# Performance work log

Measured on AMD Instinct MI355X. Metric: run time of the kernel, lower is better.

## Reference

```python
import jax, jax.numpy as jnp
import numpy as np
import math

B, S, HID = 1, 2048, 4096
HQ, HKV, D = 32, 8, 128
G = HQ // HKV          # GQA group size
OBS, W, SINK = 128, 32, 2
THETA = 500000.0
TOP_FRAC, MID_SPARSITY, LOW_FRAC = 0.05, 0.7, 0.20
K_KEEP = int(math.ceil((1.0 - MID_SPARSITY) * D))  # elements kept per level-1 token


def _rope(x):
    # x: [B, H, S, D]; standard Llama rotary embedding
    half = D // 2
    inv_freq = 1.0 / (THETA ** (jnp.arange(half, dtype=jnp.float32) / half))
    ang = jnp.arange(S, dtype=jnp.float32)[:, None] * inv_freq[None, :]  # [S, half]
    cos = jnp.concatenate([jnp.cos(ang), jnp.cos(ang)], axis=-1)  # [S, D]
    sin = jnp.concatenate([jnp.sin(ang), jnp.sin(ang)], axis=-1)
    x1, x2 = x[..., :half], x[..., half:]
    rot = jnp.concatenate([-x2, x1], axis=-1)
    return x * cos[None, None] + rot * sin[None, None]


def _topk_mask(x):
    # keep the K_KEEP largest-magnitude elements of each length-D token vector
    a = jnp.abs(x)
    thr = jnp.sort(a, axis=-1)[..., D - K_KEEP]
    return a >= thr[..., None]


def setup_inputs() -> dict:
    key = jax.random.key(0)
    ks = jax.random.split(key, 5)
    sc = HID ** -0.5
    return {
        "hidden_states": jax.random.normal(ks[0], (B, S, HID), dtype=jnp.float32),
        "wq": jax.random.normal(ks[1], (HID, HQ * D), dtype=jnp.float32) * sc,
        "wk": jax.random.normal(ks[2], (HID, HKV * D), dtype=jnp.float32) * sc,
        "wv": jax.random.normal(ks[3], (HID, HKV * D), dtype=jnp.float32) * sc,
        "wo": jax.random.normal(ks[4], (HQ * D, HID), dtype=jnp.float32) * sc,
    }


def reference(hidden_states, wq, wk, wv, wo):
    scale = 1.0 / math.sqrt(D)
    q = (hidden_states @ wq).reshape(B, S, HQ, D).transpose(0, 2, 1, 3)   # [B,HQ,S,D]
    k = (hidden_states @ wk).reshape(B, S, HKV, D).transpose(0, 2, 1, 3)  # [B,HKV,S,D]
    v = (hidden_states @ wv).reshape(B, S, HKV, D).transpose(0, 2, 1, 3)
    q, k = _rope(q), _rope(k)

    # --- observation-window GQA attention (grouped queries vs all keys) ---
    obs_q = q[:, :, S - OBS:, :].reshape(B, HKV, G, OBS, D)
    s_obs = jnp.einsum('bhgqd,bhkd->bhgqk', obs_q, k) * scale
    obs_causal = jnp.arange(S)[None, :] <= (S - OBS + jnp.arange(OBS))[:, None]  # [OBS,S]
    s_obs = jnp.where(obs_causal[None, None, None], s_obs, -jnp.inf)
    aw_kv = jax.nn.softmax(s_obs.astype(jnp.float32), axis=-1).mean(axis=2)  # [B,HKV,OBS,S]

    # per-token importance, normalized by how many obs queries observed each key
    counts = jnp.minimum(OBS, S - jnp.arange(S)).astype(jnp.float32)
    imp = aw_kv.sum(axis=2) / counts[None, None, :]  # [B,HKV,S]

    # --- global thresholds over the compressible region -> 3 sparsity levels ---
    imp_c = imp[:, :, :S - W].reshape(-1)
    t_high = jnp.quantile(imp_c, 1.0 - TOP_FRAC)
    t_low = jnp.quantile(imp_c, LOW_FRAC)
    level = jnp.where(imp >= t_high, 0, jnp.where(imp < t_low, 2, 1))
    pos = jnp.arange(S)
    dense_pos = (pos >= S - W) | (pos < SINK)     # recent window + sinks stay dense
    level = jnp.where(dense_pos[None, None, :], 0, level)

    keep_k = jnp.where((level == 0)[..., None], True, (level == 1)[..., None] & _topk_mask(k))
    keep_v = jnp.where((level == 0)[..., None], True, (level == 1)[..., None] & _topk_mask(v))
    k_sp = k * keep_k
    v_sp = v * keep_v
    evicted = level == 2

    # --- causal GQA attention over the sparsified KV cache ---
    q_g = q.reshape(B, HKV, G, S, D)
    s = jnp.einsum('bhgqd,bhkd->bhgqk', q_g, k_sp) * scale
    causal = jnp.tril(jnp.ones((S, S), dtype=bool))
    allow = causal[None, None, None] & (~evicted)[:, :, None, None, :]
    s = jnp.where(allow, s, -jnp.inf)
    p = jax.nn.softmax(s.astype(jnp.float32), axis=-1).astype(v_sp.dtype)
    o = jnp.einsum('bhgqk,bhkd->bhgqd', p, v_sp)
    o = o.reshape(B, HQ, S, D).transpose(0, 2, 1, 3).reshape(B, S, HQ * D)
    return o @ wo
```

## Files before the change

### kernel.cpp

```cpp
#include <hip/hip_runtime.h>
#include <hip/hip_bf16.h>
#include <math.h>

#define S_    2048
#define HID_  4096
#define HQ_   32
#define HKV_  8
#define D_    128
#define G_    4
#define OBS_  128
#define W_    32
#define NKV_  1024
#define NQ_   4096
#define KLD_  2048
#define SCALE_ 0.08838834764831845f
#define THR_IDX_ 89
#define NC_   16128

typedef __attribute__((ext_vector_type(4))) float f32x4;
typedef __attribute__((ext_vector_type(8))) short s16x8;
typedef __attribute__((ext_vector_type(8))) unsigned short u16x8;
typedef __attribute__((ext_vector_type(4))) unsigned short u16x4;
typedef unsigned short ushort_t;

struct TermPtrs { const ushort_t* a[6]; const ushort_t* b[6]; };
struct M1A { const ushort_t* A[3]; const ushort_t* B[3];
             const ushort_t* QA[3]; const ushort_t* QB[3]; };

__device__ __forceinline__ unsigned short f2bf(float x) {
  union { float f; unsigned u; } v; v.f = x;
  unsigned r = v.u + 0x7FFFu + ((v.u >> 16) & 1u);
  return (unsigned short)(r >> 16);
}
__device__ __forceinline__ float bf2f(unsigned short b) {
  union { unsigned u; float f; } v; v.u = ((unsigned)b) << 16;
  return v.f;
}
__device__ __forceinline__ void gload_lds16(const void* g, void* l) {
  __builtin_amdgcn_global_load_lds((const __attribute__((address_space(1))) unsigned int*)g,
                                   (__attribute__((address_space(3))) unsigned int*)l, 16, 0, 0);
}
__device__ __forceinline__ void term_sel(const TermPtrs& P, int tt,
                                         const ushort_t*& As, const ushort_t*& Bs) {
  switch (tt) {
    case 0: As = P.a[0]; Bs = P.b[0]; break;
    case 1: As = P.a[1]; Bs = P.b[1]; break;
    case 2: As = P.a[2]; Bs = P.b[2]; break;
    case 3: As = P.a[3]; Bs = P.b[3]; break;
    case 4: As = P.a[4]; Bs = P.b[4]; break;
    default: As = P.a[5]; Bs = P.b[5]; break;
  }
}
__device__ __forceinline__ void xcd_bmbn(int& bm, int& bn) {
  int nplane = gridDim.x * gridDim.y;
  int l = blockIdx.y * gridDim.x + blockIdx.x;
  int v = (l & 7) * (nplane >> 3) + (l >> 3);
  bm = v / gridDim.x;
  bn = v - bm * gridDim.x;
}

__device__ __forceinline__ void splitT_body(const float* __restrict__ src, int N,
                                            ushort_t* __restrict__ t0,
                                            ushort_t* __restrict__ t1,
                                            ushort_t* __restrict__ t2,
                                            int idx, float (*tile)[65]) {
  const int t = threadIdx.x;
  const int ntx = N >> 6;
  const int n0 = (idx % ntx) * 64, k0 = (idx / ntx) * 64;
#pragma unroll
  for (int i = 0; i < 16; ++i) {
    int s = i * 256 + t;
    int r = s >> 6, c = s & 63;
    tile[r][c] = src[(size_t)(k0 + r) * N + n0 + c];
  }
  __syncthreads();
#pragma unroll
  for (int i = 0; i < 16; ++i) {
    int s = i * 256 + t;
    int n = s >> 6, kk = s & 63;
    float x = tile[kk][n];
    unsigned short b0 = f2bf(x);
    size_t o = (size_t)(n0 + n) * HID_ + k0 + kk;
    t0[o] = b0;
    if (t1) {
      float r = x - bf2f(b0);
      unsigned short b1 = f2bf(r);
      t1[o] = b1;
      t2[o] = f2bf(r - bf2f(b1));
    }
  }
}

__global__ __launch_bounds__(256) void prep_kernel(const float* __restrict__ hid,
                                                   const float* __restrict__ wq,
                                                   const float* __restrict__ wk,
                                                   const float* __restrict__ wv,
                                                   ushort_t* h0, ushort_t* h1, ushort_t* h2,
                                                   ushort_t* wq0T, ushort_t* wq1T, ushort_t* wq2T,
                                                   ushort_t* wkv0T, ushort_t* wkv1T, ushort_t* wkv2T,
                                                   float* invf) {
  __shared__ float tile[64][65];
  const int b = blockIdx.x;
  if (b < 8192) {
    int idx = b * 256 + threadIdx.x;
    float4 v = ((const float4*)hid)[idx];
    u16x4 o0, o1, o2;
    float xs[4] = {v.x, v.y, v.z, v.w};
#pragma unroll
    for (int e = 0; e < 4; ++e) {
      float x = xs[e];
      unsigned short b0 = f2bf(x);
      float r = x - bf2f(b0);
      unsigned short b1 = f2bf(r);
      o0[e] = b0; o1[e] = b1; o2[e] = f2bf(r - bf2f(b1));
    }
    *(u16x4*)(h0 + (size_t)idx * 4) = o0;
    *(u16x4*)(h1 + (size_t)idx * 4) = o1;
    *(u16x4*)(h2 + (size_t)idx * 4) = o2;
  } else if (b < 12288) {
    splitT_body(wq, NQ_, wq0T, wq1T, wq2T, b - 8192, tile);
  } else if (b < 13312) {
    splitT_body(wk, NKV_, wkv0T, wkv1T, wkv2T, b - 12288, tile);
  } else if (b < 14336) {
    splitT_body(wv, NKV_, wkv0T + (size_t)NKV_ * HID_, wkv1T + (size_t)NKV_ * HID_,
                wkv2T + (size_t)NKV_ * HID_, b - 13312, tile);
  } else {
    int j = threadIdx.x;
    if (j < 64) invf[j] = (float)(1.0 / pow(500000.0, (double)j / 64.0));
  }
}

__global__ __launch_bounds__(256) void gemm6m(M1A P, float* __restrict__ kvp,
                                              float* __restrict__ qpart) {
  __shared__ ushort_t lds[6 * 128 * 32];
  const int t = threadIdx.x;
  const int wave = t >> 6, lane = t & 63;
  const int lc = lane & 15, lg = lane >> 4;
  const int wm = wave >> 1, wn = wave & 1;
  const int z = blockIdx.z;

  const ushort_t *As0, *As1, *As2, *Bs0, *Bs1, *Bs2;
  float* C;
  int rowA, rowB, kbeg, ksteps, N, crow0, ccol0;
  if (z < 2) {
    int bm, bn;
    xcd_bmbn(bm, bn);
    As0 = P.A[0]; As1 = P.A[1]; As2 = P.A[2];
    Bs0 = P.B[0]; Bs1 = P.B[1]; Bs2 = P.B[2];
    rowA = bm * 128; rowB = bn * 128;
    kbeg = z * 64; ksteps = 64; N = KLD_;
    C = kvp + (size_t)z * S_ * KLD_;
    crow0 = bm * 128; ccol0 = bn * 128;
  } else {
    int l = blockIdx.y * gridDim.x + blockIdx.x;
    int bn = l & 31, ks = l >> 5;
    As0 = P.QA[0]; As1 = P.QA[1]; As2 = P.QA[2];
    Bs0 = P.QB[0]; Bs1 = P.QB[1]; Bs2 = P.QB[2];
    rowA = 0; rowB = bn * 128;
    kbeg = ks * 16; ksteps = 16; N = NQ_;
    C = qpart + (size_t)ks * 128 * NQ_;
    crow0 = 0; ccol0 = bn * 128;
  }

  f32x4 acc[4][4];
#pragma unroll
  for (int fi = 0; fi < 4; ++fi)
#pragma unroll
    for (int fj = 0; fj < 4; ++fj) acc[fi][fj] = 0.f;

  for (int kb = kbeg; kb < kbeg + ksteps; ++kb) {
    __syncthreads();
#pragma unroll
    for (int ti = 0; ti < 6; ++ti) {
      const ushort_t* src = (ti == 0) ? As0 : (ti == 1) ? As1 : (ti == 2) ? As2
                          : (ti == 3) ? Bs0 : (ti == 4) ? Bs1 : Bs2;
      const int rb = (ti < 3) ? rowA : rowB;
#pragma unroll
      for (int it = 0; it < 2; ++it) {
        int slot = it * 256 + t;
        int row = slot >> 2, cp = slot & 3;
        int c = (cp - (row >> 1)) & 3;
        gload_lds16(src + (size_t)(rb + row) * HID_ + kb * 32 + c * 8,
                    lds + ti * 4096 + it * 2048 + wave * 512);
      }
    }
    __syncthreads();
    s16x8 a0[4], a1[4], a2[4], bfr[4];
#pragma unroll
    for (int f = 0; f < 4; ++f) {
      int ra = wm * 64 + f * 16 + lc;
      int ca = ((lg + (ra >> 1)) & 3) * 8;
      a0[f] = *(const s16x8*)(lds + 0 * 4096 + ra * 32 + ca);
      a1[f] = *(const s16x8*)(lds + 1 * 4096 + ra * 32 + ca);
      a2[f] = *(const s16x8*)(lds + 2 * 4096 + ra * 32 + ca);
    }
#pragma unroll
    for (int f = 0; f < 4; ++f) {
      int rb2 = wn * 64 + f * 16 + lc;
      bfr[f] = *(const s16x8*)(lds + 3 * 4096 + rb2 * 32 + (((lg + (rb2 >> 1)) & 3) * 8));
    }
#pragma unroll
    for (int fi = 0; fi < 4; ++fi)
#pragma unroll
      for (int fj = 0; fj < 4; ++fj) {
        acc[fi][fj] = __builtin_amdgcn_mfma_f32_16x16x32_bf16(a0[fi], bfr[fj], acc[fi][fj], 0, 0, 0);
        acc[fi][fj] = __builtin_amdgcn_mfma_f32_16x16x32_bf16(a1[fi], bfr[fj], acc[fi][fj], 0, 0, 0);
        acc[fi][fj] = __builtin_amdgcn_mfma_f32_16x16x32_bf16(a2[fi], bfr[fj], acc[fi][fj], 0, 0, 0);
      }
#pragma unroll
    for (int f = 0; f < 4; ++f) {
      int rb2 = wn * 64 + f * 16 + lc;
      bfr[f] = *(const s16x8*)(lds + 4 * 4096 + rb2 * 32 + (((lg + (rb2 >> 1)) & 3) * 8));
    }
#pragma unroll
    for (int fi = 0; fi < 4; ++fi)
#pragma unroll
      for (int fj = 0; fj < 4; ++fj) {
        acc[fi][fj] = __builtin_amdgcn_mfma_f32_16x16x32_bf16(a0[fi], bfr[fj], acc[fi][fj], 0, 0, 0);
        acc[fi][fj] = __builtin_amdgcn_mfma_f32_16x16x32_bf16(a1[fi], bfr[fj], acc[fi][fj], 0, 0, 0);
      }
#pragma unroll
    for (int f = 0; f < 4; ++f) {
      int rb2 = wn * 64 + f * 16 + lc;
      bfr[f] = *(const s16x8*)(lds + 5 * 4096 + rb2 * 32 + (((lg + (rb2 >> 1)) & 3) * 8));
    }
#pragma unroll
    for (int fi = 0; fi < 4; ++fi)
#pragma unroll
      for (int fj = 0; fj < 4; ++fj)
        acc[fi][fj] = __builtin_amdgcn_mfma_f32_16x16x32_bf16(a0[fi], bfr[fj], acc[fi][fj], 0, 0, 0);
  }
#pragma unroll
  for (int fi = 0; fi < 4; ++fi)
#pragma unroll
    for (int fj = 0; fj < 4; ++fj)
#pragma unroll
      for (int r = 0; r < 4; ++r)
        C[(size_t)(crow0 + wm * 64 + fi * 16 + lg * 4 + r) * N +
          ccol0 + wn * 64 + fj * 16 + lc] = acc[fi][fj][r];
}

__device__ __forceinline__ void gemm1_body(const ushort_t* __restrict__ A,
                                           const ushort_t* __restrict__ B,
                                           float* __restrict__ C,
                                           int N, int K, int KSTEPS, ushort_t* lds) {
  const int t = threadIdx.x;
  const int wave = t >> 6, lane = t & 63;
  const int lc = lane & 15, lg = lane >> 4;
  int bm, bn;
  xcd_bmbn(bm, bn);
  const int wm = wave >> 1, wn = wave & 1;
  const int srow = t >> 3, schunk = t & 7;

  f32x4 acc[4][4];
#pragma unroll
  for (int fi = 0; fi < 4; ++fi)
#pragma unroll
    for (int fj = 0; fj < 4; ++fj) acc[fi][fj] = 0.f;

  for (int kb = 0; kb < KSTEPS; ++kb) {
    __syncthreads();
#pragma unroll
    for (int g = 0; g < 4; ++g) {
      int row = g * 32 + srow;
      int sw = schunk ^ (row & 7);
      size_t co = kb * 64 + sw * 8;
      gload_lds16(A + (size_t)(bm * 128 + row) * K + co, lds + g * 2048 + wave * 512);
      gload_lds16(B + (size_t)(bn * 128 + row) * K + co, lds + 8192 + g * 2048 + wave * 512);
    }
    __syncthreads();
#pragma unroll
    for (int ks = 0; ks < 2; ++ks) {
      s16x8 af[4], bf[4];
#pragma unroll
      for (int f = 0; f < 4; ++f) {
        int ra = wm * 64 + f * 16 + lc;
        af[f] = *(const s16x8*)(lds + ra * 64 + (((ks * 4 + lg) ^ (ra & 7)) * 8));
        int rb = wn * 64 + f * 16 + lc;
        bf[f] = *(const s16x8*)(lds + 8192 + rb * 64 + (((ks * 4 + lg) ^ (rb & 7)) * 8));
      }
#pragma unroll
      for (int fi = 0; fi < 4; ++fi)
#pragma unroll
        for (int fj = 0; fj < 4; ++fj)
          acc[fi][fj] = __builtin_amdgcn_mfma_f32_16x16x32_bf16(af[fi], bf[fj], acc[fi][fj], 0, 0, 0);
    }
  }
#pragma unroll
  for (int fi = 0; fi < 4; ++fi)
#pragma unroll
    for (int fj = 0; fj < 4; ++fj)
#pragma unroll
      for (int r = 0; r < 4; ++r)
        C[(size_t)(bm * 128 + wm * 64 + fi * 16 + lg * 4 + r) * N +
          bn * 128 + wn * 64 + fj * 16 + lc] = acc[fi][fj][r];
}

__global__ __launch_bounds__(256) void gemm1(const ushort_t* __restrict__ A,
                                             const ushort_t* __restrict__ B,
                                             float* __restrict__ C,
                                             int N, int K, int KSTEPS) {
  __shared__ ushort_t lds[2 * 128 * 64];
  gemm1_body(A, B, C, N, K, KSTEPS, lds);
}

__device__ __forceinline__ void gemm_qrope_body(const ushort_t* __restrict__ A,
                                                const ushort_t* __restrict__ B,
                                                ushort_t* __restrict__ qb16,
                                                const float* __restrict__ invf,
                                                ushort_t* lds) {
  const int t = threadIdx.x;
  const int wave = t >> 6, lane = t & 63;
  const int lc = lane & 15, lg = lane >> 4;
  int bm, bn;
  xcd_bmbn(bm, bn);
  const int srow = t >> 3, schunk = t & 7;

  f32x4 acc[2][8];
#pragma unroll
  for (int f = 0; f < 2; ++f)
#pragma unroll
    for (int fj = 0; fj < 8; ++fj) acc[f][fj] = 0.f;

  for (int kb = 0; kb < 64; ++kb) {
    __syncthreads();
#pragma unroll
    for (int g = 0; g < 4; ++g) {
      int row = g * 32 + srow;
      int sw = schunk ^ (row & 7);
      size_t co = (size_t)kb * 64 + sw * 8;
      gload_lds16(A + (size_t)(bm * 128 + row) * HID_ + co, lds + g * 2048 + wave * 512);
      gload_lds16(B + (size_t)(bn * 128 + row) * HID_ + co, lds + 8192 + g * 2048 + wave * 512);
    }
    __syncthreads();
#pragma unroll
    for (int ks = 0; ks < 2; ++ks) {
      s16x8 af[2], bf[8];
#pragma unroll
      for (int f = 0; f < 2; ++f) {
        int ra = wave * 32 + f * 16 + lc;
        af[f] = *(const s16x8*)(lds + ra * 64 + (((ks * 4 + lg) ^ (ra & 7)) * 8));
      }
#pragma unroll
      for (int fj = 0; fj < 8; ++fj) {
        int rb = fj * 16 + lc;
        bf[fj] = *(const s16x8*)(lds + 8192 + rb * 64 + (((ks * 4 + lg) ^ (rb & 7)) * 8));
      }
#pragma unroll
      for (int f = 0; f < 2; ++f)
#pragma unroll
        for (int fj = 0; fj < 8; ++fj)
          acc[f][fj] = __builtin_amdgcn_mfma_f32_16x16x32_bf16(af[f], bf[fj], acc[f][fj], 0, 0, 0);
    }
  }
#pragma unroll
  for (int f = 0; f < 2; ++f)
#pragma unroll
    for (int r = 0; r < 4; ++r) {
      int row = bm * 128 + wave * 32 + f * 16 + lg * 4 + r;
      ushort_t* op = qb16 + (size_t)row * NQ_ + bn * 128;
#pragma unroll
      for (int fj = 0; fj < 4; ++fj) {
        int j = fj * 16 + lc;
        float x1 = acc[f][fj][r];
        float x2 = acc[f][fj + 4][r];
        float ang = (float)row * invf[j];
        float sn, cs; sincosf(ang, &sn, &cs);
        op[j] = f2bf(x1 * cs - x2 * sn);
        op[j + 64] = f2bf(x2 * cs + x1 * sn);
      }
    }
}

__global__ __launch_bounds__(256) void m2_kernel(const ushort_t* __restrict__ h0,
                                                 const ushort_t* __restrict__ wq0T,
                                                 ushort_t* __restrict__ qb16,
                                                 const float* __restrict__ kvp,
                                                 const float* __restrict__ invf,
                                                 float* __restrict__ kvf,
                                                 ushort_t* __restrict__ k0,
                                                 ushort_t* __restrict__ k1,
                                                 ushort_t* __restrict__ k2,
                                                 const float* __restrict__ qpart,
                                                 ushort_t* __restrict__ q0,
                                                 ushort_t* __restrict__ q1,
                                                 ushort_t* __restrict__ q2,
                                                 const float* __restrict__ wo,
                                                 ushort_t* __restrict__ woT) {
  __shared__ ushort_t lds[2 * 128 * 64];
  if (blockIdx.z == 0) {
    gemm_qrope_body(h0, wq0T, qb16, invf, lds);
    return;
  }
  const int l = blockIdx.y * gridDim.x + blockIdx.x;
  const int t = threadIdx.x;
  const size_t n = (size_t)S_ * KLD_;
  for (int vb = l; vb < 6144; vb += 512) {
    if (vb < 4096) {
      int idx = vb * 256 + t;
      int j = idx & 63;
      int h = (idx >> 6) & 7;
      int s = idx >> 9;
      size_t base = (size_t)s * KLD_ + h * 128 + j;
      float x1 = kvp[base] + kvp[base + n];
      float x2 = kvp[base + 64] + kvp[base + 64 + n];
      float ang = (float)s * invf[j];
      float sn, cs; sincosf(ang, &sn, &cs);
      float o1 = x1 * cs - x2 * sn;
      float o2 = x2 * cs + x1 * sn;
      kvf[base] = o1; kvf[base + 64] = o2;
      size_t o = (size_t)h * 262144 + (size_t)s * 128 + j;
      float ys[2] = {o1, o2};
#pragma unroll
      for (int e = 0; e < 2; ++e) {
        float x = ys[e];
        unsigned short b0 = f2bf(x);
        float r = x - bf2f(b0);
        unsigned short b1 = f2bf(r);
        k0[o + e * 64] = b0; k1[o + e * 64] = b1; k2[o + e * 64] = f2bf(r - bf2f(b1));
      }
    } else {
      int idx = (vb - 4096) * 256 + t;
      int s = idx >> 8, c4 = idx & 255;
      size_t base = (size_t)s * KLD_ + 1024 + c4 * 4;
      float4 a = *(const float4*)(kvp + base);
      float4 bb = *(const float4*)(kvp + base + n);
      float4 o;
      o.x = a.x + bb.x; o.y = a.y + bb.y; o.z = a.z + bb.z; o.w = a.w + bb.w;
      *(float4*)(kvf + base) = o;
    }
  }
  for (int vb = l; vb < 1024; vb += 512) {
    int idx = vb * 256 + t;
    int j = idx & 63;
    int hq = (idx >> 6) & 31;
    int i = idx >> 11;
    size_t base = (size_t)i * NQ_ + hq * 128 + j;
    float x1 = 0.f, x2 = 0.f;
#pragma unroll
    for (int z = 0; z < 8; ++z) {
      x1 += qpart[(size_t)z * OBS_ * NQ_ + base];
      x2 += qpart[(size_t)z * OBS_ * NQ_ + base + 64];
    }
    float ang = (float)(S_ - OBS_ + i) * invf[j];
    float sn, cs; sincosf(ang, &sn, &cs);
    float o1 = x1 * cs - x2 * sn;
    float o2 = x2 * cs + x1 * sn;
    int hk = hq >> 2, g = hq & 3;
    size_t o = (size_t)hk * 65536 + (size_t)(g * 128 + i) * 128 + j;
    float ys[2] = {o1, o2};
#pragma unroll
    for (int e = 0; e < 2; ++e) {
      float x = ys[e];
      unsigned short b0 = f2bf(x);
      float r = x - bf2f(b0);
      unsigned short b1 = f2bf(r);
      q0[o + e * 64] = b0; q1[o + e * 64] = b1; q2[o + e * 64] = f2bf(r - bf2f(b1));
    }
  }
  float (*tile)[65] = (float(*)[65])lds;
  for (int vb = l; vb < 4096; vb += 512) {
    __syncthreads();
    splitT_body(wo, HID_, woT, nullptr, nullptr, vb, tile);
  }
}

__global__ __launch_bounds__(256) void gemm6z(TermPtrs P, float* __restrict__ Cg) {
  __shared__ ushort_t lds[2 * 128 * 64];
  const int t = threadIdx.x;
  const int wave = t >> 6, lane = t & 63;
  const int lc = lane & 15, lg = lane >> 4;
  const int bm = blockIdx.y, bn = blockIdx.x, z = blockIdx.z;
  const int wm = wave >> 1, wn = wave & 1;
  const int srow = t >> 3, schunk = t & 7;
  const size_t Aoff = (size_t)z * 512 * 128;
  const size_t Boff = (size_t)z * 2048 * 128;
  float* C = Cg + (size_t)z * 512 * 2048;

  f32x4 acc[4][4];
#pragma unroll
  for (int fi = 0; fi < 4; ++fi)
#pragma unroll
    for (int fj = 0; fj < 4; ++fj) acc[fi][fj] = 0.f;

  for (int tt = 0; tt < 6; ++tt) {
    const ushort_t *As, *Bs;
    term_sel(P, tt, As, Bs);
    As += Aoff; Bs += Boff;
    for (int kb = 0; kb < 2; ++kb) {
      __syncthreads();
#pragma unroll
      for (int g = 0; g < 4; ++g) {
        int row = g * 32 + srow;
        int sw = schunk ^ (row & 7);
        gload_lds16(As + (size_t)(bm * 128 + row) * 128 + kb * 64 + sw * 8,
                    lds + g * 2048 + wave * 512);
        gload_lds16(Bs + (size_t)(bn * 128 + row) * 128 + kb * 64 + sw * 8,
                    lds + 8192 + g * 2048 + wave * 512);
      }
      __syncthreads();
#pragma unroll
      for (int ks = 0; ks < 2; ++ks) {
        s16x8 af[4], bf[4];
#pragma unroll
        for (int f = 0; f < 4; ++f) {
          int ra = wm * 64 + f * 16 + lc;
          af[f] = *(const s16x8*)(lds + ra * 64 + (((ks * 4 + lg) ^ (ra & 7)) * 8));
          int rb = wn * 64 + f * 16 + lc;
          bf[f] = *(const s16x8*)(lds + 8192 + rb * 64 + (((ks * 4 + lg) ^ (rb & 7)) * 8));
        }
#pragma unroll
        for (int fi = 0; fi < 4; ++fi)
#pragma unroll
          for (int fj = 0; fj < 4; ++fj)
            acc[fi][fj] = __builtin_amdgcn_mfma_f32_16x16x32_bf16(af[fi], bf[fj], acc[fi][fj], 0, 0, 0);
      }
    }
  }
#pragma unroll
  for (int fi = 0; fi < 4; ++fi)
#pragma unroll
    for (int fj = 0; fj < 4; ++fj)
#pragma unroll
      for (int r = 0; r < 4; ++r)
        C[(size_t)(bm * 128 + wm * 64 + fi * 16 + lg * 4 + r) * 2048 +
          bn * 128 + wn * 64 + fj * 16 + lc] = acc[fi][fj][r];
}

__global__ __launch_bounds__(256) void rowstat_kernel(const float* __restrict__ s,
                                                      float* __restrict__ mx,
                                                      float* __restrict__ dinv) {
  const int row = blockIdx.x * 4 + (threadIdx.x >> 6);
  const int lane = threadIdx.x & 63;
  const int i = row & 127;
  const int jmax = S_ - OBS_ + i;
  const float* sp = s + (size_t)row * S_;
  float vals[32];
  float m = -INFINITY;
#pragma unroll
  for (int c = 0; c < 8; ++c) {
    int j0 = c * 256 + lane * 4;
    float4 v = *(const float4*)(sp + j0);
    float e0 = (j0 + 0 <= jmax) ? v.x * SCALE_ : -INFINITY;
    float e1 = (j0 + 1 <= jmax) ? v.y * SCALE_ : -INFINITY;
    float e2 = (j0 + 2 <= jmax) ? v.z * SCALE_ : -INFINITY;
    float e3 = (j0 + 3 <= jmax) ? v.w * SCALE_ : -INFINITY;
    vals[c * 4 + 0] = e0; vals[c * 4 + 1] = e1; vals[c * 4 + 2] = e2; vals[c * 4 + 3] = e3;
    m = fmaxf(m, fmaxf(fmaxf(e0, e1), fmaxf(e2, e3)));
  }
#pragma unroll
  for (int off = 1; off < 64; off <<= 1) m = fmaxf(m, __shfl_xor(m, off, 64));
  float ssum = 0.f;
#pragma unroll
  for (int c = 0; c < 32; ++c) ssum += expf(vals[c] - m);
#pragma unroll
  for (int off = 1; off < 64; off <<= 1) ssum += __shfl_xor(ssum, off, 64);
  if (lane == 0) { mx[row] = m; dinv[row] = 1.0f / ssum; }
}

__global__ __launch_bounds__(256) void colsum_part(const float* __restrict__ s,
                                                   const float* __restrict__ mx,
                                                   const float* __restrict__ dinv,
                                                   float* __restrict__ part) {
  __shared__ float mxl[64], dvl[64];
  const int jt = blockIdx.x, hk = blockIdx.y, rc = blockIdx.z;
  const int t = threadIdx.x;
  if (t < 64) {
    mxl[t] = mx[hk * 512 + rc * 64 + t];
    dvl[t] = dinv[hk * 512 + rc * 64 + t];
  }
  __syncthreads();
  const int j = jt * 256 + t;
  const float* sp = s + ((size_t)hk * 512 + rc * 64) * S_ + j;
  float acc = 0.f;
  for (int rr = 0; rr < 64; ++rr) {
    int i = (rc * 64 + rr) & 127;
    if (j <= S_ - OBS_ + i)
      acc += expf(sp[(size_t)rr * S_] * SCALE_ - mxl[rr]) * dvl[rr];
  }
  part[((size_t)rc * 8 + hk) * S_ + j] = acc;
}

__global__ __launch_bounds__(1024) void radix_all(const float* __restrict__ part,
                                                  float* __restrict__ imp,
                                                  float* __restrict__ thr) {
  __shared__ unsigned hist[4][256];
  __shared__ unsigned pfx_s[4], need_s[4];
  const int t = threadIdx.x;
  for (int idx = t; idx < HKV_ * S_; idx += 1024) {
    int hk = idx >> 11, j = idx & 2047;
    float acc = 0.f;
#pragma unroll
    for (int rc = 0; rc < 8; ++rc) acc += part[((size_t)rc * 8 + hk) * S_ + j];
    float cnt = (float)min(OBS_, S_ - j);
    imp[idx] = acc * 0.25f / cnt;
  }
  if (t < 4) {
    pfx_s[t] = 0u;
    need_s[t] = (t == 0) ? 3225u : (t == 1) ? 3226u : (t == 2) ? 15320u : 15321u;
  }
  __syncthreads();
  for (int pass = 0; pass < 4; ++pass) {
    ((unsigned*)hist)[t] = 0u;
    __syncthreads();
    int shift = 24 - pass * 8;
    for (int idx = t; idx < NC_; idx += 1024) {
      int h = idx / (S_ - W_), j = idx - h * (S_ - W_);
      union { float f; unsigned u; } cv; cv.f = imp[h * S_ + j];
      unsigned u = cv.u;
#pragma unroll
      for (int q = 0; q < 4; ++q) {
        bool m = (pass == 0) || ((u >> (shift + 8)) == (pfx_s[q] >> (shift + 8)));
        if (m) atomicAdd(&hist[q][(u >> shift) & 255u], 1u);
      }
    }
    __syncthreads();
    if (t < 4) {
      unsigned need = need_s[t], cum = 0, pfx = pfx_s[t];
      for (int d = 0; d < 256; ++d) {
        unsigned c = hist[t][d];
        if (cum + c > need) { pfx |= ((unsigned)d) << shift; need_s[t] = need - cum; break; }
        cum += c;
      }
      pfx_s[t] = pfx;
    }
    __syncthreads();
  }
  if (t == 0) {
    union { unsigned u; float f; } c0, c1, c2, c3;
    c0.u = pfx_s[0]; c1.u = pfx_s[1]; c2.u = pfx_s[2]; c3.u = pfx_s[3];
    double fl = 0.2 * (double)(NC_ - 1) - 3225.0;
    double fh = 0.95 * (double)(NC_ - 1) - 15320.0;
    thr[0] = (float)((double)c2.f + ((double)c3.f - (double)c2.f) * fh);
    thr[1] = (float)((double)c0.f + ((double)c1.f - (double)c0.f) * fl);
  }
}

__global__ __launch_bounds__(128) void sparsify_kernel(const float* __restrict__ kv,
                                                       const float* __restrict__ imp,
                                                       const float* __restrict__ thr,
                                                       ushort_t* __restrict__ ksp,
                                                       ushort_t* __restrict__ vsp,
                                                       float* __restrict__ ebias) {
  const int b = blockIdx.x;
  const int j = b >> 3;
  const int h = b & 7;
  const int t = threadIdx.x;
  float ipv = imp[h * S_ + j];
  bool dense = (j >= S_ - W_) || (j < 2);
  int lvl = dense ? 0 : ((ipv >= thr[0]) ? 0 : ((ipv < thr[1]) ? 2 : 1));
  if (t == 0) ebias[h * S_ + j] = (lvl == 2) ? -INFINITY : 0.0f;
  __shared__ float av[128];
  __shared__ float thv;
  size_t base_in = (size_t)j * KLD_ + h * D_;
  size_t base_out = (size_t)j * NKV_ + h * D_;
  float kvv = kv[base_in + t];
  av[t] = fabsf(kvv);
  __syncthreads();
  {
    float at = av[t]; int cnt = 0;
    for (int m = 0; m < 128; ++m) { float am = av[m]; cnt += (am < at) || (am == at && m < t); }
    if (cnt == THR_IDX_) thv = at;
  }
  __syncthreads();
  {
    bool keep = (lvl == 0) || (lvl == 1 && fabsf(kvv) >= thv);
    ksp[base_out + t] = f2bf(keep ? kvv : 0.0f);
  }
  __syncthreads();
  float vvv = kv[base_in + 1024 + t];
  av[t] = fabsf(vvv);
  __syncthreads();
  {
    float at = av[t]; int cnt = 0;
    for (int m = 0; m < 128; ++m) { float am = av[m]; cnt += (am < at) || (am == at && m < t); }
    if (cnt == THR_IDX_) thv = at;
  }
  __syncthreads();
  {
    bool keep = (lvl == 0) || (lvl == 1 && fabsf(vvv) >= thv);
    vsp[base_out + t] = f2bf(keep ? vvv : 0.0f);
  }
}

__global__ __launch_bounds__(256) void vtrans_kernel(const ushort_t* __restrict__ vsp,
                                                     ushort_t* __restrict__ vspT) {
  __shared__ ushort_t tl[64][136];
  const int jt = blockIdx.x;
  const int hk = blockIdx.y;
  const int t = threadIdx.x;
#pragma unroll
  for (int i = 0; i < 4; ++i) {
    int idx = i * 256 + t;
    int j = idx >> 4, c = idx & 15;
    *(u16x8*)&tl[j][c * 8] = *(const u16x8*)(vsp + (size_t)(jt * 64 + j) * NKV_ + hk * 128 + c * 8);
  }
  __syncthreads();
  int d = t >> 1, j0 = (t & 1) * 32;
#pragma unroll
  for (int jj = 0; jj < 4; ++jj) {
    u16x8 v;
#pragma unroll
    for (int e = 0; e < 8; ++e) v[e] = tl[j0 + jj * 8 + e][d];
    *(u16x8*)(vspT + ((size_t)hk * 128 + d) * S_ + jt * 64 + j0 + jj * 8) = v;
  }
}

#define SPAD_ 66
__global__ __launch_bounds__(256) void attn_kernel(const ushort_t* __restrict__ qbp,
                                                   const ushort_t* __restrict__ ksp,
                                                   const ushort_t* __restrict__ vspT,
                                                   const float* __restrict__ ebias,
                                                   ushort_t* __restrict__ ob16) {
  __shared__ ushort_t k_lds[64 * 128];
  __shared__ ushort_t vT_lds[128 * 64];
  __shared__ float s_lds[4][16][SPAD_];
  const int b = blockIdx.x;
  const int xcd = b & 7;
  const int idx = b >> 3;
  const int h = xcd * 4 + (idx >> 4);
  const int p = idx & 15;
  const int hk = h >> 2;
  const int t = threadIdx.x;
  const int w = t >> 6, lane = t & 63;
  const int lc = lane & 15, lg = lane >> 4;

  const ushort_t* kbase = ksp + hk * D_;
  const ushort_t* vbase = vspT + (size_t)hk * D_ * S_;

  for (int strip = 0; strip < 2; ++strip) {
    const int qb = (strip == 0) ? p : 31 - p;
    const int q0 = qb * 64 + w * 16;
    s16x8 qfrag[4];
#pragma unroll
    for (int db = 0; db < 4; ++db)
      qfrag[db] = *(const s16x8*)(qbp + (size_t)(q0 + lc) * NQ_ + h * D_ + db * 32 + lg * 8);

    f32x4 o[8];
#pragma unroll
    for (int n = 0; n < 8; ++n) o[n] = 0.f;
    float mr[4] = {-INFINITY, -INFINITY, -INFINITY, -INFINITY};
    float lr[4] = {0.f, 0.f, 0.f, 0.f};

    const int ntj = qb + 1;
    for (int tj = 0; tj < ntj; ++tj) {
      const int j0 = tj * 64;
      __syncthreads();
#pragma unroll
      for (int i = 0; i < 4; ++i) {
        int slot = i * 256 + w * 64 + lane;
        int row = slot >> 4, c = slot & 15;
        const ushort_t* gp = kbase + (size_t)(j0 + row) * NKV_ + ((c ^ (row & 7)) * 8);
        gload_lds16(gp, &k_lds[(i * 256 + w * 64) * 8]);
      }
#pragma unroll
      for (int i = 0; i < 4; ++i) {
        int slot = i * 256 + w * 64 + lane;
        int d = slot >> 3, c = slot & 7;
        const ushort_t* gp = vbase + (size_t)d * S_ + j0 + ((c ^ (d & 7)) * 8);
        gload_lds16(gp, &vT_lds[(i * 256 + w * 64) * 8]);
      }
      __syncthreads();

      f32x4 sfr[4];
#pragma unroll
      for (int js = 0; js < 4; ++js) sfr[js] = 0.f;
#pragma unroll
      for (int js = 0; js < 4; ++js) {
        int row = js * 16 + lc;
#pragma unroll
        for (int db = 0; db < 4; ++db) {
          s16x8 kf = *(const s16x8*)&k_lds[row * 128 + (((db * 4 + lg) ^ (lc & 7)) * 8)];
          sfr[js] = __builtin_amdgcn_mfma_f32_16x16x32_bf16(qfrag[db], kf, sfr[js], 0, 0, 0);
        }
      }
      float eb[4];
#pragma unroll
      for (int js = 0; js < 4; ++js) eb[js] = ebias[hk * S_ + j0 + js * 16 + lc];

      const bool diag = (tj == qb);
      float sclv[4];
#pragma unroll
      for (int r = 0; r < 4; ++r) {
        float sv[4];
#pragma unroll
        for (int js = 0; js < 4; ++js) sv[js] = sfr[js][r] * SCALE_ + eb[js];
        if (diag) {
          int qrow = w * 16 + lg * 4 + r;
#pragma unroll
          for (int js = 0; js < 4; ++js)
            if (js * 16 + lc > qrow) sv[js] = -INFINITY;
        }
        float tm = fmaxf(fmaxf(sv[0], sv[1]), fmaxf(sv[2], sv[3]));
#pragma unroll
        for (int off = 1; off < 16; off <<= 1) tm = fmaxf(tm, __shfl_xor(tm, off, 64));
        float mnew = fmaxf(mr[r], tm);
        float scl = __expf(mr[r] - mnew);
        float ps = 0.f;
#pragma unroll
        for (int js = 0; js < 4; ++js) {
          float e = __expf(sv[js] - mnew);
          s_lds[w][lg * 4 + r][js * 16 + lc] = e;
          ps += e;
        }
#pragma unroll
        for (int off = 1; off < 16; off <<= 1) ps += __shfl_xor(ps, off, 64);
        lr[r] = lr[r] * scl + ps;
        mr[r] = mnew;
        sclv[r] = scl;
      }
#pragma unroll
      for (int n = 0; n < 8; ++n) {
        f32x4 ov = o[n];
#pragma unroll
        for (int r = 0; r < 4; ++r) ov[r] *= sclv[r];
        o[n] = ov;
      }
      asm volatile("s_waitcnt lgkmcnt(0)" ::: "memory");
      s16x8 pa[2];
#pragma unroll
      for (int ks = 0; ks < 2; ++ks) {
        float pv[8];
        *(f32x4*)&pv[0] = *(const f32x4*)&s_lds[w][lc][ks * 32 + lg * 8];
        *(f32x4*)&pv[4] = *(const f32x4*)&s_lds[w][lc][ks * 32 + lg * 8 + 4];
        s16x8 pk;
#pragma unroll
        for (int e = 0; e < 8; ++e) pk[e] = (short)f2bf(pv[e]);
        pa[ks] = pk;
      }
#pragma unroll
      for (int n = 0; n < 8; ++n) {
        int d = n * 16 + lc;
#pragma unroll
        for (int ks = 0; ks < 2; ++ks) {
          s16x8 vf = *(const s16x8*)&vT_lds[d * 64 + (((ks * 4 + lg) ^ (lc & 7)) * 8)];
          o[n] = __builtin_amdgcn_mfma_f32_16x16x32_bf16(pa[ks], vf, o[n], 0, 0, 0);
        }
      }
    }
#pragma unroll
    for (int r = 0; r < 4; ++r) {
      float rinv = 1.0f / lr[r];
      int row = q0 + lg * 4 + r;
#pragma unroll
      for (int n = 0; n < 8; ++n)
        ob16[(size_t)row * NQ_ + h * D_ + n * 16 + lc] = f2bf(o[n][r] * rinv);
    }
  }
}

extern "C" void kernel_launch(void* const* d_in, const int* in_sizes, int n_in,
                              void* d_out, int out_size, void* d_ws, size_t ws_size,
                              hipStream_t stream) {
  (void)in_sizes; (void)n_in; (void)out_size; (void)ws_size;
  const float* hid = (const float*)d_in[0];
  const float* wq  = (const float*)d_in[1];
  const float* wk  = (const float*)d_in[2];
  const float* wv  = (const float*)d_in[3];
  const float* wo  = (const float*)d_in[4];
  float* out = (float*)d_out;
  char* ws = (char*)d_ws;
  const size_t MB = 1ull << 20;

  ushort_t* h0     = (ushort_t*)(ws + 0 * MB);
  ushort_t* h1     = (ushort_t*)(ws + 16 * MB);
  ushort_t* h2     = (ushort_t*)(ws + 32 * MB);
  ushort_t* wq0T   = (ushort_t*)(ws + 48 * MB);
  ushort_t* wq1T   = (ushort_t*)(ws + 80 * MB);
  ushort_t* wq2T   = (ushort_t*)(ws + 112 * MB);
  ushort_t* wkv0T  = (ushort_t*)(ws + 144 * MB);
  ushort_t* wkv1T  = (ushort_t*)(ws + 160 * MB);
  ushort_t* wkv2T  = (ushort_t*)(ws + 176 * MB);
  float*    kvp    = (float*)d_out;
  float*    qpart  = (float*)(ws + 192 * MB);
  float*    kvf    = (float*)(ws + 112 * MB);
  ushort_t* qb16   = (ushort_t*)(ws + 16 * MB);
  ushort_t* kb0    = (ushort_t*)(ws + 32 * MB);
  ushort_t* kb1    = (ushort_t*)(ws + 36 * MB);
  ushort_t* kb2    = (ushort_t*)(ws + 40 * MB);
  float*    s_obs  = (float*)(ws + 48 * MB);
  ushort_t* woT    = (ushort_t*)(ws + 144 * MB);
  ushort_t* ksp    = (ushort_t*)(ws + 176 * MB);
  ushort_t* vsp    = (ushort_t*)(ws + 180 * MB);
  ushort_t* vspT   = (ushort_t*)(ws + 184 * MB);
  ushort_t* ob16   = (ushort_t*)(ws + 188 * MB + 512 * 1024);
  ushort_t* qo0    = (ushort_t*)(ws + 208 * MB);
  ushort_t* qo1    = (ushort_t*)(ws + 209 * MB);
  ushort_t* qo2    = (ushort_t*)(ws + 210 * MB);
  char*     misc   = ws + 212 * MB;
  float*    impv   = (float*)(misc + 0);
  float*    eb     = (float*)(misc + 64 * 1024);
  float*    invf   = (float*)(misc + 128 * 1024);
  float*    thr    = (float*)(misc + 132 * 1024);
  float*    part   = (float*)(misc + 256 * 1024);
  float*    mxbuf  = (float*)(misc + 1024 * 1024);
  float*    dinvb  = (float*)(misc + 1088 * 1024);

  prep_kernel<<<14337, 256, 0, stream>>>(hid, wq, wk, wv, h0, h1, h2,
                                         wq0T, wq1T, wq2T, wkv0T, wkv1T, wkv2T, invf);

  const size_t obs_off = (size_t)(S_ - OBS_) * HID_;
  {
    M1A P;
    P.A[0] = h0; P.A[1] = h1; P.A[2] = h2;
    P.B[0] = wkv0T; P.B[1] = wkv1T; P.B[2] = wkv2T;
    P.QA[0] = h0 + obs_off; P.QA[1] = h1 + obs_off; P.QA[2] = h2 + obs_off;
    P.QB[0] = wq0T; P.QB[1] = wq1T; P.QB[2] = wq2T;
    gemm6m<<<dim3(16, 16, 3), 256, 0, stream>>>(P, kvp, qpart);
  }

  m2_kernel<<<dim3(32, 16, 2), 256, 0, stream>>>(h0, wq0T, qb16, kvp, invf, kvf,
                                                 kb0, kb1, kb2, qpart, qo0, qo1, qo2,
                                                 wo, woT);

  {
    TermPtrs P;
    P.a[0] = qo0; P.b[0] = kb0;
    P.a[1] = qo0; P.b[1] = kb1;
    P.a[2] = qo1; P.b[2] = kb0;
    P.a[3] = qo1; P.b[3] = kb1;
    P.a[4] = qo0; P.b[4] = kb2;
    P.a[5] = qo2; P.b[5] = kb0;
    gemm6z<<<dim3(16, 4, 8), 256, 0, stream>>>(P, s_obs);
  }

  rowstat_kernel<<<1024, 256, 0, stream>>>(s_obs, mxbuf, dinvb);
  colsum_part<<<dim3(8, 8, 8), 256, 0, stream>>>(s_obs, mxbuf, dinvb, part);
  radix_all<<<1, 1024, 0, stream>>>(part, impv, thr);

  sparsify_kernel<<<S_ * HKV_, 128, 0, stream>>>(kvf, impv, thr, ksp, vsp, eb);
  vtrans_kernel<<<dim3(S_ / 64, HKV_), 256, 0, stream>>>(vsp, vspT);
  attn_kernel<<<512, 256, 0, stream>>>(qb16, ksp, vspT, eb, ob16);

  gemm1<<<dim3(32, 16, 1), 256, 0, stream>>>(ob16, woT, out, HID_, HID_, 64);
}
```

Measured before the change: 812.5 us.

## Move Q projection+RoPE into gemm6m, drop KV split-K, add MFMA priority hints

The Q projection with RoPE moves out of the second kernel and into the first GEMM launch as extra z-slices, so it runs alongside the KV projection. The KV GEMM no longer splits K across two partial buffers; each block does the full reduction, which removes the partial-sum add and the V-copy pass in the finish kernel. Sparsify now reads V straight from the projection output, and qb16 is placed in the output buffer. The attention kernel wraps its MFMA loops in s_setprio hints. The risk is load imbalance from longer KV blocks mixed with the much heavier Q blocks in one grid.

After: 832.0 us. 1.02x slower.

```diff
diff --git a/kernel.cpp b/kernel.cpp
--- a/kernel.cpp
+++ b/kernel.cpp
@@ -131,25 +131,90 @@
 }
 
 __global__ __launch_bounds__(256) void gemm6m(M1A P, float* __restrict__ kvp,
-                                              float* __restrict__ qpart) {
+                                              float* __restrict__ qpart,
+                                              ushort_t* __restrict__ qb16,
+                                              const float* __restrict__ invf) {
   __shared__ ushort_t lds[6 * 128 * 32];
   const int t = threadIdx.x;
   const int wave = t >> 6, lane = t & 63;
   const int lc = lane & 15, lg = lane >> 4;
+  const int z = blockIdx.z;
+
+  if (z >= 2) {
+    int tid = (z - 2) * 256 + blockIdx.y * gridDim.x + blockIdx.x;
+    int v = (tid & 7) * 64 + (tid >> 3);
+    int bm = v >> 5, bn = v & 31;
+    const ushort_t* A = P.A[0];
+    const ushort_t* B = P.QB[0];
+    const int srow = t >> 3, schunk = t & 7;
+    f32x4 acc[2][8];
+#pragma unroll
+    for (int f = 0; f < 2; ++f)
+#pragma unroll
+      for (int fj = 0; fj < 8; ++fj) acc[f][fj] = 0.f;
+    for (int kb = 0; kb < 64; ++kb) {
+      __syncthreads();
+#pragma unroll
+      for (int g = 0; g < 4; ++g) {
+        int row = g * 32 + srow;
+        int sw = schunk ^ (row & 7);
+        size_t co = (size_t)kb * 64 + sw * 8;
+        gload_lds16(A + (size_t)(bm * 128 + row) * HID_ + co, lds + g * 2048 + wave * 512);
+        gload_lds16(B + (size_t)(bn * 128 + row) * HID_ + co, lds + 8192 + g * 2048 + wave * 512);
+      }
+      __syncthreads();
+#pragma unroll
+      for (int ks = 0; ks < 2; ++ks) {
+        s16x8 af[2], bf[8];
+#pragma unroll
+        for (int f = 0; f < 2; ++f) {
+          int ra = wave * 32 + f * 16 + lc;
+          af[f] = *(const s16x8*)(lds + ra * 64 + (((ks * 4 + lg) ^ (ra & 7)) * 8));
+        }
+#pragma unroll
+        for (int fj = 0; fj < 8; ++fj) {
+          int rb = fj * 16 + lc;
+          bf[fj] = *(const s16x8*)(lds + 8192 + rb * 64 + (((ks * 4 + lg) ^ (rb & 7)) * 8));
+        }
+#pragma unroll
+        for (int f = 0; f < 2; ++f)
+#pragma unroll
+          for (int fj = 0; fj < 8; ++fj)
+            acc[f][fj] = __builtin_amdgcn_mfma_f32_16x16x32_bf16(af[f], bf[fj], acc[f][fj], 0, 0, 0);
+      }
+    }
+#pragma unroll
+    for (int f = 0; f < 2; ++f)
+#pragma unroll
+      for (int r = 0; r < 4; ++r) {
+        int row = bm * 128 + wave * 32 + f * 16 + lg * 4 + r;
+        ushort_t* op = qb16 + (size_t)row * NQ_ + bn * 128;
+#pragma unroll
+        for (int fj = 0; fj < 4; ++fj) {
+          int j = fj * 16 + lc;
+          float x1 = acc[f][fj][r];
+          float x2 = acc[f][fj + 4][r];
+          float ang = (float)row * invf[j];
+          float sn, cs; sincosf(ang, &sn, &cs);
+          op[j] = f2bf(x1 * cs - x2 * sn);
+          op[j + 64] = f2bf(x2 * cs + x1 * sn);
+        }
+      }
+    return;
+  }
+
   const int wm = wave >> 1, wn = wave & 1;
-  const int z = blockIdx.z;
-
   const ushort_t *As0, *As1, *As2, *Bs0, *Bs1, *Bs2;
   float* C;
   int rowA, rowB, kbeg, ksteps, N, crow0, ccol0;
-  if (z < 2) {
+  if (z == 0) {
     int bm, bn;
     xcd_bmbn(bm, bn);
     As0 = P.A[0]; As1 = P.A[1]; As2 = P.A[2];
     Bs0 = P.B[0]; Bs1 = P.B[1]; Bs2 = P.B[2];
     rowA = bm * 128; rowB = bn * 128;
-    kbeg = z * 64; ksteps = 64; N = KLD_;
-    C = kvp + (size_t)z * S_ * KLD_;
+    kbeg = 0; ksteps = 128; N = KLD_;
+    C = kvp;
     crow0 = bm * 128; ccol0 = bn * 128;
   } else {
     int l = blockIdx.y * gridDim.x + blockIdx.x;
@@ -240,10 +305,11 @@
           ccol0 + wn * 64 + fj * 16 + lc] = acc[fi][fj][r];
 }
 
-__device__ __forceinline__ void gemm1_body(const ushort_t* __restrict__ A,
-                                           const ushort_t* __restrict__ B,
-                                           float* __restrict__ C,
-                                           int N, int K, int KSTEPS, ushort_t* lds) {
+__global__ __launch_bounds__(256) void gemm1(const ushort_t* __restrict__ A,
+                                             const ushort_t* __restrict__ B,
+                                             float* __restrict__ C,
+                                             int N, int K, int KSTEPS) {
+  __shared__ ushort_t lds[2 * 128 * 64];
   const int t = threadIdx.x;
   const int wave = t >> 6, lane = t & 63;
   const int lc = lane & 15, lg = lane >> 4;
@@ -296,138 +362,43 @@
           bn * 128 + wn * 64 + fj * 16 + lc] = acc[fi][fj][r];
 }
 
-__global__ __launch_bounds__(256) void gemm1(const ushort_t* __restrict__ A,
-                                             const ushort_t* __restrict__ B,
-                                             float* __restrict__ C,
-                                             int N, int K, int KSTEPS) {
-  __shared__ ushort_t lds[2 * 128 * 64];
-  gemm1_body(A, B, C, N, K, KSTEPS, lds);
-}
-
-__device__ __forceinline__ void gemm_qrope_body(const ushort_t* __restrict__ A,
-                                                const ushort_t* __restrict__ B,
-                                                ushort_t* __restrict__ qb16,
-                                                const float* __restrict__ invf,
-                                                ushort_t* lds) {
-  const int t = threadIdx.x;
-  const int wave = t >> 6, lane = t & 63;
-  const int lc = lane & 15, lg = lane >> 4;
-  int bm, bn;
-  xcd_bmbn(bm, bn);
-  const int srow = t >> 3, schunk = t & 7;
-
-  f32x4 acc[2][8];
-#pragma unroll
-  for (int f = 0; f < 2; ++f)
-#pragma unroll
-    for (int fj = 0; fj < 8; ++fj) acc[f][fj] = 0.f;
-
-  for (int kb = 0; kb < 64; ++kb) {
-    __syncthreads();
-#pragma unroll
-    for (int g = 0; g < 4; ++g) {
-      int row = g * 32 + srow;
-      int sw = schunk ^ (row & 7);
-      size_t co = (size_t)kb * 64 + sw * 8;
-      gload_lds16(A + (size_t)(bm * 128 + row) * HID_ + co, lds + g * 2048 + wave * 512);
-      gload_lds16(B + (size_t)(bn * 128 + row) * HID_ + co, lds + 8192 + g * 2048 + wave * 512);
-    }
-    __syncthreads();
-#pragma unroll
-    for (int ks = 0; ks < 2; ++ks) {
-      s16x8 af[2], bf[8];
-#pragma unroll
-      for (int f = 0; f < 2; ++f) {
-        int ra = wave * 32 + f * 16 + lc;
-        af[f] = *(const s16x8*)(lds + ra * 64 + (((ks * 4 + lg) ^ (ra & 7)) * 8));
-      }
-#pragma unroll
-      for (int fj = 0; fj < 8; ++fj) {
-        int rb = fj * 16 + lc;
-        bf[fj] = *(const s16x8*)(lds + 8192 + rb * 64 + (((ks * 4 + lg) ^ (rb & 7)) * 8));
-      }
-#pragma unroll
-      for (int f = 0; f < 2; ++f)
-#pragma unroll
-        for (int fj = 0; fj < 8; ++fj)
-          acc[f][fj] = __builtin_amdgcn_mfma_f32_16x16x32_bf16(af[f], bf[fj], acc[f][fj], 0, 0, 0);
-    }
-  }
-#pragma unroll
-  for (int f = 0; f < 2; ++f)
-#pragma unroll
-    for (int r = 0; r < 4; ++r) {
-      int row = bm * 128 + wave * 32 + f * 16 + lg * 4 + r;
-      ushort_t* op = qb16 + (size_t)row * NQ_ + bn * 128;
-#pragma unroll
-      for (int fj = 0; fj < 4; ++fj) {
-        int j = fj * 16 + lc;
-        float x1 = acc[f][fj][r];
-        float x2 = acc[f][fj + 4][r];
-        float ang = (float)row * invf[j];
-        float sn, cs; sincosf(ang, &sn, &cs);
-        op[j] = f2bf(x1 * cs - x2 * sn);
-        op[j + 64] = f2bf(x2 * cs + x1 * sn);
-      }
-    }
-}
-
-__global__ __launch_bounds__(256) void m2_kernel(const ushort_t* __restrict__ h0,
-                                                 const ushort_t* __restrict__ wq0T,
-                                                 ushort_t* __restrict__ qb16,
-                                                 const float* __restrict__ kvp,
-                                                 const float* __restrict__ invf,
-                                                 float* __restrict__ kvf,
-                                                 ushort_t* __restrict__ k0,
-                                                 ushort_t* __restrict__ k1,
-                                                 ushort_t* __restrict__ k2,
-                                                 const float* __restrict__ qpart,
-                                                 ushort_t* __restrict__ q0,
-                                                 ushort_t* __restrict__ q1,
-                                                 ushort_t* __restrict__ q2,
-                                                 const float* __restrict__ wo,
-                                                 ushort_t* __restrict__ woT) {
-  __shared__ ushort_t lds[2 * 128 * 64];
-  if (blockIdx.z == 0) {
-    gemm_qrope_body(h0, wq0T, qb16, invf, lds);
-    return;
-  }
+__global__ __launch_bounds__(256) void finish_kernel(const float* __restrict__ kvp,
+                                                     const float* __restrict__ invf,
+                                                     float* __restrict__ kvf,
+                                                     ushort_t* __restrict__ k0,
+                                                     ushort_t* __restrict__ k1,
+                                                     ushort_t* __restrict__ k2,
+                                                     const float* __restrict__ qpart,
+                                                     ushort_t* __restrict__ q0,
+                                                     ushort_t* __restrict__ q1,
+                                                     ushort_t* __restrict__ q2,
+                                                     const float* __restrict__ wo,
+                                                     ushort_t* __restrict__ woT) {
+  __shared__ float tile[64][65];
   const int l = blockIdx.y * gridDim.x + blockIdx.x;
   const int t = threadIdx.x;
-  const size_t n = (size_t)S_ * KLD_;
-  for (int vb = l; vb < 6144; vb += 512) {
-    if (vb < 4096) {
-      int idx = vb * 256 + t;
-      int j = idx & 63;
-      int h = (idx >> 6) & 7;
-      int s = idx >> 9;
-      size_t base = (size_t)s * KLD_ + h * 128 + j;
-      float x1 = kvp[base] + kvp[base + n];
-      float x2 = kvp[base + 64] + kvp[base + 64 + n];
-      float ang = (float)s * invf[j];
-      float sn, cs; sincosf(ang, &sn, &cs);
-      float o1 = x1 * cs - x2 * sn;
-      float o2 = x2 * cs + x1 * sn;
-      kvf[base] = o1; kvf[base + 64] = o2;
-      size_t o = (size_t)h * 262144 + (size_t)s * 128 + j;
-      float ys[2] = {o1, o2};
-#pragma unroll
-      for (int e = 0; e < 2; ++e) {
-        float x = ys[e];
-        unsigned short b0 = f2bf(x);
-        float r = x - bf2f(b0);
-        unsigned short b1 = f2bf(r);
-        k0[o + e * 64] = b0; k1[o + e * 64] = b1; k2[o + e * 64] = f2bf(r - bf2f(b1));
-      }
-    } else {
-      int idx = (vb - 4096) * 256 + t;
-      int s = idx >> 8, c4 = idx & 255;
-      size_t base = (size_t)s * KLD_ + 1024 + c4 * 4;
-      float4 a = *(const float4*)(kvp + base);
-      float4 bb = *(const float4*)(kvp + base + n);
-      float4 o;
-      o.x = a.x + bb.x; o.y = a.y + bb.y; o.z = a.z + bb.z; o.w = a.w + bb.w;
-      *(float4*)(kvf + base) = o;
+  for (int vb = l; vb < 4096; vb += 512) {
+    int idx = vb * 256 + t;
+    int j = idx & 63;
+    int h = (idx >> 6) & 7;
+    int s = idx >> 9;
+    size_t base = (size_t)s * KLD_ + h * 128 + j;
+    float x1 = kvp[base];
+    float x2 = kvp[base + 64];
+    float ang = (float)s * invf[j];
+    float sn, cs; sincosf(ang, &sn, &cs);
+    float o1 = x1 * cs - x2 * sn;
+    float o2 = x2 * cs + x1 * sn;
+    kvf[base] = o1; kvf[base + 64] = o2;
+    size_t o = (size_t)h * 262144 + (size_t)s * 128 + j;
+    float ys[2] = {o1, o2};
+#pragma unroll
+    for (int e = 0; e < 2; ++e) {
+      float x = ys[e];
+      unsigned short b0 = f2bf(x);
+      float r = x - bf2f(b0);
+      unsigned short b1 = f2bf(r);
+      k0[o + e * 64] = b0; k1[o + e * 64] = b1; k2[o + e * 64] = f2bf(r - bf2f(b1));
     }
   }
   for (int vb = l; vb < 1024; vb += 512) {
@@ -458,7 +429,6 @@
       q0[o + e * 64] = b0; q1[o + e * 64] = b1; q2[o + e * 64] = f2bf(r - bf2f(b1));
     }
   }
-  float (*tile)[65] = (float(*)[65])lds;
   for (int vb = l; vb < 4096; vb += 512) {
     __syncthreads();
     splitT_body(wo, HID_, woT, nullptr, nullptr, vb, tile);
@@ -636,7 +606,8 @@
   }
 }
 
-__global__ __launch_bounds__(128) void sparsify_kernel(const float* __restrict__ kv,
+__global__ __launch_bounds__(128) void sparsify_kernel(const float* __restrict__ kvK,
+                                                       const float* __restrict__ kvV,
                                                        const float* __restrict__ imp,
                                                        const float* __restrict__ thr,
                                                        ushort_t* __restrict__ ksp,
@@ -654,7 +625,7 @@
   __shared__ float thv;
   size_t base_in = (size_t)j * KLD_ + h * D_;
   size_t base_out = (size_t)j * NKV_ + h * D_;
-  float kvv = kv[base_in + t];
+  float kvv = kvK[base_in + t];
   av[t] = fabsf(kvv);
   __syncthreads();
   {
@@ -668,7 +639,7 @@
     ksp[base_out + t] = f2bf(keep ? kvv : 0.0f);
   }
   __syncthreads();
-  float vvv = kv[base_in + 1024 + t];
+  float vvv = kvV[base_in + 1024 + t];
   av[t] = fabsf(vvv);
   __syncthreads();
   {
@@ -765,6 +736,7 @@
       f32x4 sfr[4];
 #pragma unroll
       for (int js = 0; js < 4; ++js) sfr[js] = 0.f;
+      __builtin_amdgcn_s_setprio(1);
 #pragma unroll
       for (int js = 0; js < 4; ++js) {
         int row = js * 16 + lc;
@@ -774,6 +746,7 @@
           sfr[js] = __builtin_amdgcn_mfma_f32_16x16x32_bf16(qfrag[db], kf, sfr[js], 0, 0, 0);
         }
       }
+      __builtin_amdgcn_s_setprio(0);
       float eb[4];
 #pragma unroll
       for (int js = 0; js < 4; ++js) eb[js] = ebias[hk * S_ + j0 + js * 16 + lc];
@@ -828,6 +801,7 @@
         for (int e = 0; e < 8; ++e) pk[e] = (short)f2bf(pv[e]);
         pa[ks] = pk;
       }
+      __builtin_amdgcn_s_setprio(1);
 #pragma unroll
       for (int n = 0; n < 8; ++n) {
         int d = n * 16 + lc;
@@ -837,6 +811,7 @@
           o[n] = __builtin_amdgcn_mfma_f32_16x16x32_bf16(pa[ks], vf, o[n], 0, 0, 0);
         }
       }
+      __builtin_amdgcn_s_setprio(0);
     }
 #pragma unroll
     for (int r = 0; r < 4; ++r) {
@@ -872,9 +847,9 @@
   ushort_t* wkv1T  = (ushort_t*)(ws + 160 * MB);
   ushort_t* wkv2T  = (ushort_t*)(ws + 176 * MB);
   float*    kvp    = (float*)d_out;
+  ushort_t* qb16   = (ushort_t*)((char*)d_out + (size_t)S_ * KLD_ * 4);
   float*    qpart  = (float*)(ws + 192 * MB);
   float*    kvf    = (float*)(ws + 112 * MB);
-  ushort_t* qb16   = (ushort_t*)(ws + 16 * MB);
   ushort_t* kb0    = (ushort_t*)(ws + 32 * MB);
   ushort_t* kb1    = (ushort_t*)(ws + 36 * MB);
   ushort_t* kb2    = (ushort_t*)(ws + 40 * MB);
@@ -906,12 +881,11 @@
     P.B[0] = wkv0T; P.B[1] = wkv1T; P.B[2] = wkv2T;
     P.QA[0] = h0 + obs_off; P.QA[1] = h1 + obs_off; P.QA[2] = h2 + obs_off;
     P.QB[0] = wq0T; P.QB[1] = wq1T; P.QB[2] = wq2T;
-    gemm6m<<<dim3(16, 16, 3), 256, 0, stream>>>(P, kvp, qpart);
-  }
-
-  m2_kernel<<<dim3(32, 16, 2), 256, 0, stream>>>(h0, wq0T, qb16, kvp, invf, kvf,
-                                                 kb0, kb1, kb2, qpart, qo0, qo1, qo2,
-                                                 wo, woT);
+    gemm6m<<<dim3(16, 16, 4), 256, 0, stream>>>(P, kvp, qpart, qb16, invf);
+  }
+
+  finish_kernel<<<dim3(32, 16, 1), 256, 0, stream>>>(kvp, invf, kvf, kb0, kb1, kb2,
+                                                     qpart, qo0, qo1, qo2, wo, woT);
 
   {
     TermPtrs P;
@@ -928,7 +902,7 @@
   colsum_part<<<dim3(8, 8, 8), 256, 0, stream>>>(s_obs, mxbuf, dinvb, part);
   radix_all<<<1, 1024, 0, stream>>>(part, impv, thr);
 
-  sparsify_kernel<<<S_ * HKV_, 128, 0, stream>>>(kvf, impv, thr, ksp, vsp, eb);
+  sparsify_kernel<<<S_ * HKV_, 128, 0, stream>>>(kvf, kvp, impv, thr, ksp, vsp, eb);
   vtrans_kernel<<<dim3(S_ / 64, HKV_), 256, 0, stream>>>(vsp, vspT);
   attn_kernel<<<512, 256, 0, stream>>>(qb16, ksp, vspT, eb, ob16);
 
```
